# Kernel optimization log

Measured on AMD Instinct MI355X. Metric: run time of the kernel, lower is better.

The kernel has to match this reference:

```python
import jax, jax.numpy as jnp
import numpy as np

V, E, H, L, F, NQ, C = 32000, 256, 8, 4, 1024, 256, 10
B, S = 8, 1024
DK = E // H


def setup_inputs() -> dict:
    key = jax.random.key(0)
    ks = jax.random.split(key, 10)
    f = lambda k, shape, s=0.02: jax.random.normal(k, shape, jnp.float32) * s
    return {
        'tokens': jax.random.randint(ks[0], (B, S), 0, V, jnp.int32),
        'emb': f(ks[1], (V, E), 1.0),
        'theta_attn': f(ks[2], (L, H, DK), 0.5),
        'Wc': f(ks[3], (L, E, E)),
        'bc': jnp.zeros((L, E), jnp.float32),
        'g1': jnp.ones((L, E), jnp.float32),
        'bn1': jnp.zeros((L, E), jnp.float32),
        'theta_ffn': f(ks[4], (L, NQ), 0.5),
        'W1': f(ks[5], (L, NQ, F)),
        'b1': jnp.zeros((L, F), jnp.float32),
        'W2': f(ks[6], (L, F, E)),
        'b2': jnp.zeros((L, E), jnp.float32),
        'g2': jnp.ones((L, E), jnp.float32),
        'bn2': jnp.zeros((L, E), jnp.float32),
        'Wcls': f(ks[7], (E, C)),
        'bcls': jnp.zeros((C,), jnp.float32),
    }


def _ln(x, g, b, eps=1e-5):
    m = x.mean(-1, keepdims=True)
    v = ((x - m) ** 2).mean(-1, keepdims=True)
    return (x - m) / jnp.sqrt(v + eps) * g + b


def _pos_encoding(seq, dim):
    pos = jnp.arange(seq, dtype=jnp.float32)[:, None]
    div = jnp.exp(jnp.arange(0, dim, 2, dtype=jnp.float32) * (-np.log(10000.0) / dim))
    pe = jnp.zeros((seq, dim), jnp.float32)
    pe = pe.at[:, 0::2].set(jnp.sin(pos * div)).at[:, 1::2].set(jnp.cos(pos * div))
    return pe


def _qattn_proj(xh, theta):
    # xh: [B,S,H,dk], theta: [H,dk]. Circuit RX(x+th) per wire, CNOT ring, <Z_i>.
    # Analytic: <Z_i> = prod_{j<=i} cos(phi_j) for i>=1; <Z_0> = prod_{j>=1} cos(phi_j)
    c = jnp.cos(xh + theta)              # [B,S,H,dk]
    cum = jnp.cumprod(c, axis=-1)        # cum[...,i] = prod_{j<=i} c_j
    head0 = jnp.prod(c[..., 1:], axis=-1, keepdims=True)
    return jnp.concatenate([head0, cum[..., 1:]], axis=-1)  # [B,S,H,dk]


def _forward(tokens, emb, theta_attn, Wc, bc, g1, bn1, theta_ffn, W1, b1, W2, b2, g2, bn2, Wcls, bcls):
    b, s = tokens.shape
    x = emb[tokens] + _pos_encoding(s, E)  # [B,S,E]
    scale = 1.0 / np.sqrt(DK)
    for l in range(L):
        # quantum multi-head projection; q = k = v (same deterministic circuit)
        xh = x.reshape(b, s, H, DK)
        p = _qattn_proj(xh, theta_attn[l]).reshape(b, s, E)
        scores = jax.nn.softmax(jnp.einsum('bqe,bke->bqk', p, p) * scale, axis=-1)
        attn = jnp.einsum('bqk,bke->bqe', scores, p) @ Wc[l] + bc[l]
        x = _ln(x + attn, g1[l], bn1[l])
        # quantum FFN: <Z_i> = cos(x_i) * cos(theta_i), NQ == E here
        q = jnp.cos(x[..., :NQ]) * jnp.cos(theta_ffn[l])
        f = jax.nn.relu(q @ W1[l] + b1[l]) @ W2[l] + b2[l]
        x = _ln(x + f, g2[l], bn2[l])
    return x.mean(axis=1) @ Wcls + bcls  # [B,C]


def reference(tokens, emb, theta_attn, Wc, bc, g1, bn1, theta_ffn, W1, b1, W2, b2, g2, bn2, Wcls, bcls):
    return _forward(tokens, emb, theta_attn, Wc, bc, g1, bn1, theta_ffn, W1, b1, W2, b2, g2, bn2, Wcls, bcls)
```

## Files before the change

kernel.cpp:

```cpp
#include <hip/hip_runtime.h>
#include <hip/hip_bf16.h>
#include <math.h>

#define BB 8
#define SS 1024
#define EE 256
#define HH 8
#define DKK 32
#define LL 4
#define FF 1024
#define NQQ 256
#define CC 10

typedef __attribute__((ext_vector_type(8))) short short8;
typedef __attribute__((ext_vector_type(4))) short s16x4;
typedef __attribute__((ext_vector_type(4))) float f32x4;

static __device__ __forceinline__ f32x4 mfma16(short8 a, short8 b, f32x4 c) {
    return __builtin_amdgcn_mfma_f32_16x16x32_bf16(a, b, c, 0, 0, 0);
}
static __device__ __forceinline__ short f2bf(float f) {
    __hip_bfloat16 h = __float2bfloat16(f);
    return *reinterpret_cast<short*>(&h);
}

#define FRAG(P, tile, KG, kg, l) ((P) + (((size_t)((tile)*(KG) + (kg)))*64 + (l))*8)

static __device__ __forceinline__ void qproj_row(
        const float* __restrict__ xrow,
        const float* __restrict__ th,
        int b, int s, int h,
        short* __restrict__ PQ, short* __restrict__ PT) {
    float v[DKK];
    float cum = __cosf(xrow[h * DKK + 0] + th[0]);
    float prod1 = 1.0f;
    #pragma unroll
    for (int j = 1; j < DKK; ++j) {
        float c = __cosf(xrow[h * DKK + j] + th[j]);
        cum *= c;
        prod1 *= c;
        v[j] = cum;
    }
    v[0] = prod1;
    short* pq = PQ + (size_t)b * SS * EE;
    int stile = s >> 4, lr = s & 15;
    #pragma unroll
    for (int lg = 0; lg < 4; ++lg) {
        short8 u;
        #pragma unroll
        for (int j = 0; j < 8; ++j) u[j] = f2bf(v[lg*8 + j]);
        *(short8*)FRAG(pq, stile*8 + h, 1, 0, lg*16 + lr) = u;
    }
    short* pt = PT + (size_t)b * SS * EE;
    int kt = s >> 5, lgs = (s >> 3) & 3, j0 = s & 7;
    #pragma unroll
    for (int j = 0; j < DKK; ++j) {
        int e = h * DKK + j;
        FRAG(pt, e >> 4, 32, kt, lgs*16 + (e & 15))[j0] = f2bf(v[j]);
    }
}

__global__ __launch_bounds__(512) void k_embedq(
        const int* __restrict__ tokens, const float* __restrict__ emb,
        const float* __restrict__ theta_q,
        float* __restrict__ x, short* __restrict__ PQ, short* __restrict__ PT) {
    const int t = threadIdx.x;
    const int bsw = blockIdx.x & 7, local = blockIdx.x >> 3;
    const int tok0 = bsw * SS + local * 32;
    __shared__ float xls[32 * 268];
    {
        int r = t >> 4, c0 = (t & 15) * 16;
        int bs = tok0 + r;
        int s  = bs & (SS - 1);
        int tok = tokens[bs];
        const float* er = emb + (size_t)tok * EE + c0;
        float vals[16];
        #pragma unroll
        for (int i = 0; i < 16; ++i) {
            int col = c0 + i;
            int i2 = col >> 1;
            float div = __expf(-(float)(2 * i2) * (logf(10000.0f) / (float)EE));
            float ang = (float)s * div;
            float pe = (col & 1) ? __cosf(ang) : __sinf(ang);
            vals[i] = er[i] + pe;
            xls[r * 268 + col] = vals[i];
        }
        float* xg = x + (size_t)bs * EE + c0;
        #pragma unroll
        for (int i4 = 0; i4 < 4; ++i4)
            *(float4*)(xg + i4 * 4) = *(const float4*)&vals[i4 * 4];
    }
    __syncthreads();
    if (t < 256) {
        int sl = t >> 3, h = t & 7;
        int bs = tok0 + sl;
        qproj_row(&xls[sl * 268], theta_q + h * DKK,
                  bs >> 10, bs & (SS - 1), h, PQ, PT);
    }
}

__global__ __launch_bounds__(256) void k_trall(
        const float* __restrict__ W1, const float* __restrict__ W2,
        const float* __restrict__ Wc,
        short* __restrict__ W1P, short* __restrict__ W2P, short* __restrict__ WcP) {
    int bid = blockIdx.x;
    int lyr = bid / 576, rem = bid % 576;
    const float* in; short* out; int R, C, tile;
    if (rem < 256)      { in = W1 + (size_t)lyr*NQQ*FF; out = W1P + (size_t)lyr*FF*NQQ; R = NQQ; C = FF;  tile = rem; }
    else if (rem < 512) { in = W2 + (size_t)lyr*FF*EE;  out = W2P + (size_t)lyr*EE*FF;  R = FF;  C = EE;  tile = rem - 256; }
    else                { in = Wc + (size_t)lyr*EE*EE;  out = WcP + (size_t)lyr*EE*EE;  R = EE;  C = EE;  tile = rem - 512; }
    const int KG = R >> 5;
    int tiles_c = C >> 5;
    int tc = tile % tiles_c, tr = tile / tiles_c;
    __shared__ float tl[32][33];
    int t = threadIdx.x;
    int rr = t >> 5, cc = t & 31;
    #pragma unroll
    for (int i = 0; i < 4; ++i)
        tl[rr + i*8][cc] = in[(size_t)(tr*32 + rr + i*8) * C + tc*32 + cc];
    __syncthreads();
    int ro = t >> 3, co = (t & 7) * 4;
    int n = tc*32 + ro;
    int k = tr*32 + co;
    int ntile = n >> 4, lr = n & 15;
    int kg = k >> 5, lg = (k & 31) >> 3, j0 = k & 7;
    s16x4 v;
    v[0] = f2bf(tl[co + 0][ro]);
    v[1] = f2bf(tl[co + 1][ro]);
    v[2] = f2bf(tl[co + 2][ro]);
    v[3] = f2bf(tl[co + 3][ro]);
    *(s16x4*)(FRAG(out, ntile, KG, kg, lg*16 + lr) + j0) = v;
}

__global__ __launch_bounds__(256) void k_attn7(const short* __restrict__ PQ,
                                               const short* __restrict__ PT,
                                               short* __restrict__ YP) {
    const int b   = blockIdx.x & 7;
    const int qt  = blockIdx.x >> 3;
    const int tid = threadIdx.x;
    const int w   = tid >> 6;
    const int l   = tid & 63;
    const int lr  = l & 15, lg = l >> 4;
    const short* pq = PQ + (size_t)b * SS * EE;
    const short* pt = PT + (size_t)b * SS * EE;

    __shared__ float accP[2][16][264];
    __shared__ float lsL[4][16];
    __shared__ short wlds[4][16 * 40];

    short8 qf[8];
    #pragma unroll
    for (int kg = 0; kg < 8; ++kg)
        qf[kg] = *(const short8*)FRAG(pq, qt*8 + kg, 1, 0, l);

    f32x4 acc[16];
    #pragma unroll
    for (int i = 0; i < 16; ++i) acc[i] = f32x4{0.f, 0.f, 0.f, 0.f};
    float ls[4] = {0.f, 0.f, 0.f, 0.f};
    const float scale = 0.17677669529663687f;
    short* wl = wlds[w];

    for (int i = 0; i < 8; ++i) {
        const int kt = w + 4 * i;
        short8 sb0[8], sb1[8];
        #pragma unroll
        for (int kg = 0; kg < 8; ++kg) {
            sb0[kg] = *(const short8*)FRAG(pq, (2*kt)*8   + kg, 1, 0, l);
            sb1[kg] = *(const short8*)FRAG(pq, (2*kt+1)*8 + kg, 1, 0, l);
        }
        f32x4 s0a = {0.f,0.f,0.f,0.f}, s0b = {0.f,0.f,0.f,0.f};
        f32x4 s1a = {0.f,0.f,0.f,0.f}, s1b = {0.f,0.f,0.f,0.f};
        #pragma unroll
        for (int kg = 0; kg < 4; ++kg) {
            s0a = mfma16(qf[kg], sb0[kg], s0a);
            s1a = mfma16(qf[kg], sb1[kg], s1a);
        }
        #pragma unroll
        for (int kg = 4; kg < 8; ++kg) {
            s0b = mfma16(qf[kg], sb0[kg], s0b);
            s1b = mfma16(qf[kg], sb1[kg], s1b);
        }
        short8 pvb0[8];
        #pragma unroll
        for (int nt = 0; nt < 8; ++nt)
            pvb0[nt] = *(const short8*)FRAG(pt, nt, 32, kt, l);

        #pragma unroll
        for (int r = 0; r < 4; ++r) {
            float p0 = __expf((s0a[r] + s0b[r]) * scale);
            float p1 = __expf((s1a[r] + s1b[r]) * scale);
            ls[r] += p0 + p1;
            int q = lg * 4 + r;
            wl[q * 40 + lr]      = f2bf(p0);
            wl[q * 40 + 16 + lr] = f2bf(p1);
        }
        short8 pa = *(const short8*)(wl + lr * 40 + lg * 8);
        short8 pvb1[8];
        #pragma unroll
        for (int nt = 0; nt < 8; ++nt)
            pvb1[nt] = *(const short8*)FRAG(pt, 8 + nt, 32, kt, l);
        #pragma unroll
        for (int nt = 0; nt < 8; ++nt)
            acc[nt] = mfma16(pa, pvb0[nt], acc[nt]);
        #pragma unroll
        for (int nt = 0; nt < 8; ++nt)
            acc[8 + nt] = mfma16(pa, pvb1[nt], acc[8 + nt]);
    }

    #pragma unroll
    for (int r = 0; r < 4; ++r) {
        ls[r] += __shfl_xor(ls[r], 1);
        ls[r] += __shfl_xor(ls[r], 2);
        ls[r] += __shfl_xor(ls[r], 4);
        ls[r] += __shfl_xor(ls[r], 8);
    }
    if (lr == 0) {
        #pragma unroll
        for (int r = 0; r < 4; ++r)
            lsL[w][lg * 4 + r] = ls[r];
    }

    if (w >= 2) {
        #pragma unroll
        for (int nt = 0; nt < 16; ++nt)
            #pragma unroll
            for (int r = 0; r < 4; ++r)
                accP[w - 2][lg * 4 + r][nt * 16 + lr] = acc[nt][r];
    }
    __syncthreads();
    if (w < 2) {
        #pragma unroll
        for (int nt = 0; nt < 16; ++nt)
            #pragma unroll
            for (int r = 0; r < 4; ++r)
                accP[w][lg * 4 + r][nt * 16 + lr] += acc[nt][r];
    }
    __syncthreads();

    const int q = tid >> 4, c = tid & 15;
    float L = lsL[0][q] + lsL[1][q] + lsL[2][q] + lsL[3][q];
    float inv = 1.0f / L;
    short ov[16];
    #pragma unroll
    for (int j = 0; j < 4; ++j) {
        float4 a  = *(const float4*)&accP[0][q][c * 16 + j * 4];
        float4 bb = *(const float4*)&accP[1][q][c * 16 + j * 4];
        ov[j*4 + 0] = f2bf((a.x + bb.x) * inv);
        ov[j*4 + 1] = f2bf((a.y + bb.y) * inv);
        ov[j*4 + 2] = f2bf((a.z + bb.z) * inv);
        ov[j*4 + 3] = f2bf((a.w + bb.w) * inv);
    }
    short* yb = YP + (size_t)b * SS * EE;
    int kgo = c >> 1, lgo = (c & 1) * 2;
    *(short8*)FRAG(yb, qt*8 + kgo, 1, 0, lgo*16 + q)     = *(const short8*)&ov[0];
    *(short8*)FRAG(yb, qt*8 + kgo, 1, 0, (lgo+1)*16 + q) = *(const short8*)&ov[8];
}

__global__ __launch_bounds__(512) void k_wcffnq(
        const short* __restrict__ YP, const short* __restrict__ WcP,
        const float* __restrict__ bc, const float* __restrict__ g1,
        const float* __restrict__ bn1,
        const float* __restrict__ tf, const short* __restrict__ W1P,
        const float* __restrict__ b1, const short* __restrict__ W2P,
        const float* __restrict__ b2, const float* __restrict__ g2,
        const float* __restrict__ bn2,
        float* __restrict__ x,
        const float* __restrict__ theta_q, short* __restrict__ PQ,
        short* __restrict__ PT, int has_next) {
    const int t = threadIdx.x, w = t >> 6, l = t & 63;
    const int lr = l & 15, lg = l >> 4;
    const int wg = w >> 2, wn = w & 3;
    const int b = blockIdx.x & 7;
    const int local = blockIdx.x >> 3;
    const int tok0 = b * SS + local * 32;
    const int qt0 = local * 2;

    __shared__ __align__(16) char smem[34304 + 16384 + 16384];
    float* outw = (float*)smem;
    char*  qls  = smem + 34304;
    char*  hls  = smem + 34304 + 16384;
    float* fout = (float*)(smem + 34304);

    const short* yb = YP + (size_t)b * SS * EE;

    {
        short8 af[8];
        #pragma unroll
        for (int kg = 0; kg < 8; ++kg)
            af[kg] = *(const short8*)FRAG(yb, (qt0 + wg)*8 + kg, 1, 0, l);
        f32x4 acc[4];
        #pragma unroll
        for (int i = 0; i < 4; ++i) acc[i] = f32x4{0.f,0.f,0.f,0.f};
        #pragma unroll
        for (int nt = 0; nt < 4; ++nt) {
            #pragma unroll
            for (int kg = 0; kg < 8; ++kg) {
                short8 bv = *(const short8*)FRAG(WcP, wn*4 + nt, 8, kg, l);
                acc[nt] = mfma16(af[kg], bv, acc[nt]);
            }
        }
        #pragma unroll
        for (int nt = 0; nt < 4; ++nt) {
            int e = wn * 64 + nt * 16 + lr;
            float bce = bc[e];
            #pragma unroll
            for (int r = 0; r < 4; ++r)
                outw[(wg*16 + lg*4 + r) * 268 + e] = acc[nt][r] + bce;
        }
    }
    __syncthreads();

    #pragma unroll
    for (int j = 0; j < 4; ++j) {
        int q = w * 4 + j;
        float4 v  = *(float4*)&outw[q * 268 + l * 4];
        float4 xv = *(const float4*)(x + (size_t)(tok0 + q) * EE + l * 4);
        v.x += xv.x; v.y += xv.y; v.z += xv.z; v.w += xv.w;
        float s = v.x + v.y + v.z + v.w;
        for (int off = 32; off > 0; off >>= 1) s += __shfl_xor(s, off);
        float mean = s * (1.0f / EE);
        float4 d;
        d.x = v.x - mean; d.y = v.y - mean; d.z = v.z - mean; d.w = v.w - mean;
        float s2 = d.x*d.x + d.y*d.y + d.z*d.z + d.w*d.w;
        for (int off = 32; off > 0; off >>= 1) s2 += __shfl_xor(s2, off);
        float inv = rsqrtf(s2 * (1.0f / EE) + 1e-5f);
        float4 gv  = *(const float4*)(g1  + l * 4);
        float4 bnv = *(const float4*)(bn1 + l * 4);
        float4 o;
        o.x = d.x * inv * gv.x + bnv.x;
        o.y = d.y * inv * gv.y + bnv.y;
        o.z = d.z * inv * gv.z + bnv.z;
        o.w = d.w * inv * gv.w + bnv.w;
        *(float4*)&outw[q * 268 + l * 4] = o;
        float4 tv = *(const float4*)(tf + l * 4);
        float q0 = __cosf(o.x) * __cosf(tv.x);
        float q1 = __cosf(o.y) * __cosf(tv.y);
        float q2 = __cosf(o.z) * __cosf(tv.z);
        float q3 = __cosf(o.w) * __cosf(tv.w);
        int byte = (q * 512 + l * 8) ^ ((q & 7) << 4);
        *(unsigned*)(qls + byte) =
            (unsigned)(unsigned short)f2bf(q0) | ((unsigned)(unsigned short)f2bf(q1) << 16);
        *(unsigned*)(qls + byte + 4) =
            (unsigned)(unsigned short)f2bf(q2) | ((unsigned)(unsigned short)f2bf(q3) << 16);
    }
    __syncthreads();

    f32x4 acc2[2][2];
    #pragma unroll
    for (int mt = 0; mt < 2; ++mt)
        #pragma unroll
        for (int nt = 0; nt < 2; ++nt) acc2[mt][nt] = f32x4{0.f,0.f,0.f,0.f};

    for (int fc = 0; fc < 4; ++fc) {
        f32x4 acc1[2][2];
        #pragma unroll
        for (int mt = 0; mt < 2; ++mt)
            #pragma unroll
            for (int i = 0; i < 2; ++i) acc1[mt][i] = f32x4{0.f,0.f,0.f,0.f};
        #pragma unroll
        for (int kg = 0; kg < 8; ++kg) {
            int ca = (kg*32 + lg*8) * 2;
            short8 a0 = *(const short8*)(qls + ((lr*512      + ca) ^ ((lr & 7) << 4)));
            short8 a1 = *(const short8*)(qls + (((16+lr)*512 + ca) ^ ((lr & 7) << 4)));
            #pragma unroll
            for (int i = 0; i < 2; ++i) {
                short8 bv = *(const short8*)FRAG(W1P, fc*16 + w*2 + i, 8, kg, l);
                acc1[0][i] = mfma16(a0, bv, acc1[0][i]);
                acc1[1][i] = mfma16(a1, bv, acc1[1][i]);
            }
        }
        #pragma unroll
        for (int mt = 0; mt < 2; ++mt) {
            #pragma unroll
            for (int i = 0; i < 2; ++i) {
                int fg   = (fc*16 + w*2 + i) * 16 + lr;
                int fcol = (w*2 + i) * 16 + lr;
                float bb = b1[fg];
                #pragma unroll
                for (int r = 0; r < 4; ++r) {
                    int tq = mt * 16 + lg * 4 + r;
                    float hv = fmaxf(acc1[mt][i][r] + bb, 0.0f);
                    int byte = (tq * 512 + fcol * 2) ^ ((tq & 7) << 4);
                    *(short*)(hls + byte) = f2bf(hv);
                }
            }
        }
        __syncthreads();
        #pragma unroll
        for (int k8 = 0; k8 < 8; ++k8) {
            int ca = (k8*32 + lg*8) * 2;
            short8 h0 = *(const short8*)(hls + ((lr*512      + ca) ^ ((lr & 7) << 4)));
            short8 h1 = *(const short8*)(hls + (((16+lr)*512 + ca) ^ ((lr & 7) << 4)));
            #pragma unroll
            for (int nt = 0; nt < 2; ++nt) {
                short8 bv = *(const short8*)FRAG(W2P, w*2 + nt, 32, fc*8 + k8, l);
                acc2[0][nt] = mfma16(h0, bv, acc2[0][nt]);
                acc2[1][nt] = mfma16(h1, bv, acc2[1][nt]);
            }
        }
        __syncthreads();
    }

    #pragma unroll
    for (int mt = 0; mt < 2; ++mt) {
        #pragma unroll
        for (int nt = 0; nt < 2; ++nt) {
            int e = (w*2 + nt) * 16 + lr;
            float b2e = b2[e];
            #pragma unroll
            for (int r = 0; r < 4; ++r)
                fout[(mt*16 + lg*4 + r) * 256 + e] = acc2[mt][nt][r] + b2e;
        }
    }
    __syncthreads();

    #pragma unroll
    for (int j = 0; j < 4; ++j) {
        int q = w * 4 + j;
        float4 v  = *(float4*)&fout[q * 256 + l * 4];
        float4 x1 = *(float4*)&outw[q * 268 + l * 4];
        v.x += x1.x; v.y += x1.y; v.z += x1.z; v.w += x1.w;
        float s = v.x + v.y + v.z + v.w;
        for (int off = 32; off > 0; off >>= 1) s += __shfl_xor(s, off);
        float mean = s * (1.0f / EE);
        float4 d;
        d.x = v.x - mean; d.y = v.y - mean; d.z = v.z - mean; d.w = v.w - mean;
        float s2 = d.x*d.x + d.y*d.y + d.z*d.z + d.w*d.w;
        for (int off = 32; off > 0; off >>= 1) s2 += __shfl_xor(s2, off);
        float inv = rsqrtf(s2 * (1.0f / EE) + 1e-5f);
        float4 gv  = *(const float4*)(g2  + l * 4);
        float4 bnv = *(const float4*)(bn2 + l * 4);
        float4 o;
        o.x = d.x * inv * gv.x + bnv.x;
        o.y = d.y * inv * gv.y + bnv.y;
        o.z = d.z * inv * gv.z + bnv.z;
        o.w = d.w * inv * gv.w + bnv.w;
        *(float4*)(x + (size_t)(tok0 + q) * EE + l * 4) = o;
        *(float4*)&outw[q * 268 + l * 4] = o;
    }
    __syncthreads();

    if (has_next && t < 256) {
        int sl = t >> 3, h = t & 7;
        int bs = tok0 + sl;
        qproj_row(&outw[sl * 268], theta_q + h * DKK,
                  bs >> 10, bs & (SS - 1), h, PQ, PT);
    }
}

__global__ __launch_bounds__(256) void k_head1(const float* __restrict__ x,
                                               float* __restrict__ hpart) {
    int b = blockIdx.x & 7, ch = blockIdx.x >> 3;
    int t = threadIdx.x;
    float acc = 0.0f;
    #pragma unroll 8
    for (int s = ch * 32; s < ch * 32 + 32; ++s)
        acc += x[((size_t)b * SS + s) * EE + t];
    hpart[(size_t)(b * 32 + ch) * EE + t] = acc;
}

__global__ __launch_bounds__(256) void k_head2(const float* __restrict__ hpart,
                                               const float* __restrict__ Wcls,
                                               const float* __restrict__ bcls,
                                               float* __restrict__ out) {
    int b = blockIdx.x;
    int t = threadIdx.x;
    __shared__ float xm[EE];
    float acc = 0.0f;
    #pragma unroll 8
    for (int j = 0; j < 32; ++j)
        acc += hpart[(size_t)(b * 32 + j) * EE + t];
    xm[t] = acc * (1.0f / (float)SS);
    __syncthreads();
    if (t < CC) {
        float a = bcls[t];
        #pragma unroll 8
        for (int e = 0; e < EE; ++e) a += xm[e] * Wcls[e * CC + t];
        out[b * CC + t] = a;
    }
}

extern "C" void kernel_launch(void* const* d_in, const int* in_sizes, int n_in,
                              void* d_out, int out_size, void* d_ws, size_t ws_size,
                              hipStream_t stream) {
    (void)in_sizes; (void)n_in; (void)out_size; (void)ws_size;
    const int*   tokens     = (const int*)d_in[0];
    const float* emb        = (const float*)d_in[1];
    const float* theta_attn = (const float*)d_in[2];
    const float* Wc         = (const float*)d_in[3];
    const float* bc         = (const float*)d_in[4];
    const float* g1         = (const float*)d_in[5];
    const float* bn1        = (const float*)d_in[6];
    const float* theta_ffn  = (const float*)d_in[7];
    const float* W1         = (const float*)d_in[8];
    const float* b1         = (const float*)d_in[9];
    const float* W2         = (const float*)d_in[10];
    const float* b2         = (const float*)d_in[11];
    const float* g2         = (const float*)d_in[12];
    const float* bn2        = (const float*)d_in[13];
    const float* Wcls       = (const float*)d_in[14];
    const float* bcls       = (const float*)d_in[15];
    float* out = (float*)d_out;

    const size_t nTok = (size_t)BB * SS * EE;
    float* x     = (float*)d_ws;
    short* PQ    = (short*)(x + nTok);
    short* PT    = PQ  + nTok;
    short* YP    = PT  + nTok;
    short* W1P   = YP  + nTok;
    short* W2P   = W1P + (size_t)LL * FF * NQQ;
    short* WcP   = W2P + (size_t)LL * EE * FF;
    float* hpart = (float*)(WcP + (size_t)LL * EE * EE);

    k_embedq<<<(BB * SS) / 32, 512, 0, stream>>>(tokens, emb, theta_attn, x, PQ, PT);
    k_trall<<<LL * 576, 256, 0, stream>>>(W1, W2, Wc, W1P, W2P, WcP);

    for (int l = 0; l < LL; ++l) {
        int has_next = (l + 1 < LL) ? 1 : 0;
        const float* thq = theta_attn + (size_t)(has_next ? l + 1 : 0) * HH * DKK;
        k_attn7<<<BB * 64, 256, 0, stream>>>(PQ, PT, YP);
        k_wcffnq<<<(BB * SS) / 32, 512, 0, stream>>>(
            YP, WcP + (size_t)l * EE * EE, bc + (size_t)l * EE,
            g1 + (size_t)l * EE, bn1 + (size_t)l * EE,
            theta_ffn + (size_t)l * NQQ,
            W1P + (size_t)l * FF * NQQ, b1 + (size_t)l * FF,
            W2P + (size_t)l * EE * FF, b2 + (size_t)l * EE,
            g2 + (size_t)l * EE, bn2 + (size_t)l * EE,
            x, thq, PQ, PT, has_next);
    }

    k_head1<<<BB * 32, 256, 0, stream>>>(x, hpart);
    k_head2<<<BB, 256, 0, stream>>>(hpart, Wcls, bcls, out);
}
```

Measured before the change: 248.4 us.

## Merge prep kernels, double-buffer attention K loads, fuse mean-pool into last layer

Merges the embedding/projection kernel and the weight-transpose kernel into one launch, with the embedding part now handling 16 tokens per 256-thread block. The attention loop is unrolled through a macro that prefetches the next key tile's fragments into alternate register buffers while the current tile is computed, and it loads the PV fragments inline. The last layer's FFN kernel computes the per-chunk sequence partial sums from shared memory and skips writing x, which removes the separate head1 kernel. The double buffering raises register pressure in the attention kernel, which could lower occupancy.

```diff
diff --git a/kernel.cpp b/kernel.cpp
--- a/kernel.cpp
+++ b/kernel.cpp
@@ -60,77 +60,117 @@
     }
 }
 
-__global__ __launch_bounds__(512) void k_embedq(
+__global__ __launch_bounds__(256) void k_prep(
+        const float* __restrict__ W1, const float* __restrict__ W2,
+        const float* __restrict__ Wc,
+        short* __restrict__ W1P, short* __restrict__ W2P, short* __restrict__ WcP,
         const int* __restrict__ tokens, const float* __restrict__ emb,
         const float* __restrict__ theta_q,
         float* __restrict__ x, short* __restrict__ PQ, short* __restrict__ PT) {
+    __shared__ float shmem[16 * 268];
     const int t = threadIdx.x;
-    const int bsw = blockIdx.x & 7, local = blockIdx.x >> 3;
-    const int tok0 = bsw * SS + local * 32;
-    __shared__ float xls[32 * 268];
-    {
-        int r = t >> 4, c0 = (t & 15) * 16;
-        int bs = tok0 + r;
-        int s  = bs & (SS - 1);
-        int tok = tokens[bs];
-        const float* er = emb + (size_t)tok * EE + c0;
-        float vals[16];
-        #pragma unroll
-        for (int i = 0; i < 16; ++i) {
-            int col = c0 + i;
-            int i2 = col >> 1;
-            float div = __expf(-(float)(2 * i2) * (logf(10000.0f) / (float)EE));
-            float ang = (float)s * div;
-            float pe = (col & 1) ? __cosf(ang) : __sinf(ang);
-            vals[i] = er[i] + pe;
-            xls[r * 268 + col] = vals[i];
-        }
-        float* xg = x + (size_t)bs * EE + c0;
-        #pragma unroll
-        for (int i4 = 0; i4 < 4; ++i4)
-            *(float4*)(xg + i4 * 4) = *(const float4*)&vals[i4 * 4];
-    }
-    __syncthreads();
-    if (t < 256) {
-        int sl = t >> 3, h = t & 7;
-        int bs = tok0 + sl;
-        qproj_row(&xls[sl * 268], theta_q + h * DKK,
-                  bs >> 10, bs & (SS - 1), h, PQ, PT);
-    }
-}
-
-__global__ __launch_bounds__(256) void k_trall(
-        const float* __restrict__ W1, const float* __restrict__ W2,
-        const float* __restrict__ Wc,
-        short* __restrict__ W1P, short* __restrict__ W2P, short* __restrict__ WcP) {
-    int bid = blockIdx.x;
-    int lyr = bid / 576, rem = bid % 576;
-    const float* in; short* out; int R, C, tile;
-    if (rem < 256)      { in = W1 + (size_t)lyr*NQQ*FF; out = W1P + (size_t)lyr*FF*NQQ; R = NQQ; C = FF;  tile = rem; }
-    else if (rem < 512) { in = W2 + (size_t)lyr*FF*EE;  out = W2P + (size_t)lyr*EE*FF;  R = FF;  C = EE;  tile = rem - 256; }
-    else                { in = Wc + (size_t)lyr*EE*EE;  out = WcP + (size_t)lyr*EE*EE;  R = EE;  C = EE;  tile = rem - 512; }
-    const int KG = R >> 5;
-    int tiles_c = C >> 5;
-    int tc = tile % tiles_c, tr = tile / tiles_c;
-    __shared__ float tl[32][33];
-    int t = threadIdx.x;
-    int rr = t >> 5, cc = t & 31;
-    #pragma unroll
-    for (int i = 0; i < 4; ++i)
-        tl[rr + i*8][cc] = in[(size_t)(tr*32 + rr + i*8) * C + tc*32 + cc];
-    __syncthreads();
-    int ro = t >> 3, co = (t & 7) * 4;
-    int n = tc*32 + ro;
-    int k = tr*32 + co;
-    int ntile = n >> 4, lr = n & 15;
-    int kg = k >> 5, lg = (k & 31) >> 3, j0 = k & 7;
-    s16x4 v;
-    v[0] = f2bf(tl[co + 0][ro]);
-    v[1] = f2bf(tl[co + 1][ro]);
-    v[2] = f2bf(tl[co + 2][ro]);
-    v[3] = f2bf(tl[co + 3][ro]);
-    *(s16x4*)(FRAG(out, ntile, KG, kg, lg*16 + lr) + j0) = v;
-}
+    if (blockIdx.x < 2304) {
+        int bid = blockIdx.x;
+        int lyr = bid / 576, rem = bid % 576;
+        const float* in; short* out; int R, C, tile;
+        if (rem < 256)      { in = W1 + (size_t)lyr*NQQ*FF; out = W1P + (size_t)lyr*FF*NQQ; R = NQQ; C = FF;  tile = rem; }
+        else if (rem < 512) { in = W2 + (size_t)lyr*FF*EE;  out = W2P + (size_t)lyr*EE*FF;  R = FF;  C = EE;  tile = rem - 256; }
+        else                { in = Wc + (size_t)lyr*EE*EE;  out = WcP + (size_t)lyr*EE*EE;  R = EE;  C = EE;  tile = rem - 512; }
+        const int KG = R >> 5;
+        int tiles_c = C >> 5;
+        int tc = tile % tiles_c, tr = tile / tiles_c;
+        float (*tl)[33] = (float(*)[33])shmem;
+        int rr = t >> 5, cc = t & 31;
+        #pragma unroll
+        for (int i = 0; i < 4; ++i)
+            tl[rr + i*8][cc] = in[(size_t)(tr*32 + rr + i*8) * C + tc*32 + cc];
+        __syncthreads();
+        int ro = t >> 3, co = (t & 7) * 4;
+        int n = tc*32 + ro;
+        int k = tr*32 + co;
+        int ntile = n >> 4, lr = n & 15;
+        int kg = k >> 5, lg = (k & 31) >> 3, j0 = k & 7;
+        s16x4 v;
+        v[0] = f2bf(tl[co + 0][ro]);
+        v[1] = f2bf(tl[co + 1][ro]);
+        v[2] = f2bf(tl[co + 2][ro]);
+        v[3] = f2bf(tl[co + 3][ro]);
+        *(s16x4*)(FRAG(out, ntile, KG, kg, lg*16 + lr) + j0) = v;
+    } else {
+        int blk = blockIdx.x - 2304;
+        int bsw = blk & 7, local = blk >> 3;
+        int tok0 = bsw * SS + local * 16;
+        {
+            int r = t >> 4, c0 = (t & 15) * 16;
+            int bs = tok0 + r;
+            int s  = bs & (SS - 1);
+            int tok = tokens[bs];
+            const float* er = emb + (size_t)tok * EE + c0;
+            float vals[16];
+            #pragma unroll
+            for (int i = 0; i < 16; ++i) {
+                int col = c0 + i;
+                int i2 = col >> 1;
+                float div = __expf(-(float)(2 * i2) * (logf(10000.0f) / (float)EE));
+                float ang = (float)s * div;
+                float pe = (col & 1) ? __cosf(ang) : __sinf(ang);
+                vals[i] = er[i] + pe;
+                shmem[r * 268 + col] = vals[i];
+            }
+            float* xg = x + (size_t)bs * EE + c0;
+            #pragma unroll
+            for (int i4 = 0; i4 < 4; ++i4)
+                *(float4*)(xg + i4 * 4) = *(const float4*)&vals[i4 * 4];
+        }
+        __syncthreads();
+        if (t < 128) {
+            int sl = t >> 3, h = t & 7;
+            int bs = tok0 + sl;
+            qproj_row(&shmem[sl * 268], theta_q + h * DKK,
+                      bs >> 10, bs & (SS - 1), h, PQ, PT);
+        }
+    }
+}
+
+#define ATTN_STEP(I, C0, C1, N0, N1)                                          \
+    {                                                                         \
+        const int kt = w + 4 * (I);                                           \
+        if ((I) < 7) {                                                        \
+            const int ktn = kt + 4;                                           \
+            _Pragma("unroll")                                                 \
+            for (int kg = 0; kg < 8; ++kg) {                                  \
+                N0[kg] = *(const short8*)FRAG(pq, (2*ktn)*8   + kg, 1, 0, l); \
+                N1[kg] = *(const short8*)FRAG(pq, (2*ktn+1)*8 + kg, 1, 0, l); \
+            }                                                                 \
+        }                                                                     \
+        f32x4 s0a = {0.f,0.f,0.f,0.f}, s0b = {0.f,0.f,0.f,0.f};               \
+        f32x4 s1a = {0.f,0.f,0.f,0.f}, s1b = {0.f,0.f,0.f,0.f};               \
+        _Pragma("unroll")                                                     \
+        for (int kg = 0; kg < 4; ++kg) {                                      \
+            s0a = mfma16(qf[kg], C0[kg], s0a);                                \
+            s1a = mfma16(qf[kg], C1[kg], s1a);                                \
+        }                                                                     \
+        _Pragma("unroll")                                                     \
+        for (int kg = 4; kg < 8; ++kg) {                                      \
+            s0b = mfma16(qf[kg], C0[kg], s0b);                                \
+            s1b = mfma16(qf[kg], C1[kg], s1b);                                \
+        }                                                                     \
+        _Pragma("unroll")                                                     \
+        for (int r = 0; r < 4; ++r) {                                         \
+            float p0 = __expf((s0a[r] + s0b[r]) * scale);                     \
+            float p1 = __expf((s1a[r] + s1b[r]) * scale);                     \
+            ls[r] += p0 + p1;                                                 \
+            int qq = lg * 4 + r;                                              \
+            wl[qq * 40 + lr]      = f2bf(p0);                                 \
+            wl[qq * 40 + 16 + lr] = f2bf(p1);                                 \
+        }                                                                     \
+        short8 pa = *(const short8*)(wl + lr * 40 + lg * 8);                  \
+        _Pragma("unroll")                                                     \
+        for (int nt = 0; nt < 16; ++nt) {                                     \
+            short8 bv = *(const short8*)FRAG(pt, nt, 32, kt, l);              \
+            acc[nt] = mfma16(pa, bv, acc[nt]);                                \
+        }                                                                     \
+    }
 
 __global__ __launch_bounds__(256) void k_attn7(const short* __restrict__ PQ,
                                                const short* __restrict__ PT,
@@ -160,52 +200,21 @@
     const float scale = 0.17677669529663687f;
     short* wl = wlds[w];
 
-    for (int i = 0; i < 8; ++i) {
-        const int kt = w + 4 * i;
-        short8 sb0[8], sb1[8];
-        #pragma unroll
-        for (int kg = 0; kg < 8; ++kg) {
-            sb0[kg] = *(const short8*)FRAG(pq, (2*kt)*8   + kg, 1, 0, l);
-            sb1[kg] = *(const short8*)FRAG(pq, (2*kt+1)*8 + kg, 1, 0, l);
-        }
-        f32x4 s0a = {0.f,0.f,0.f,0.f}, s0b = {0.f,0.f,0.f,0.f};
-        f32x4 s1a = {0.f,0.f,0.f,0.f}, s1b = {0.f,0.f,0.f,0.f};
-        #pragma unroll
-        for (int kg = 0; kg < 4; ++kg) {
-            s0a = mfma16(qf[kg], sb0[kg], s0a);
-            s1a = mfma16(qf[kg], sb1[kg], s1a);
-        }
-        #pragma unroll
-        for (int kg = 4; kg < 8; ++kg) {
-            s0b = mfma16(qf[kg], sb0[kg], s0b);
-            s1b = mfma16(qf[kg], sb1[kg], s1b);
-        }
-        short8 pvb0[8];
-        #pragma unroll
-        for (int nt = 0; nt < 8; ++nt)
-            pvb0[nt] = *(const short8*)FRAG(pt, nt, 32, kt, l);
-
-        #pragma unroll
-        for (int r = 0; r < 4; ++r) {
-            float p0 = __expf((s0a[r] + s0b[r]) * scale);
-            float p1 = __expf((s1a[r] + s1b[r]) * scale);
-            ls[r] += p0 + p1;
-            int q = lg * 4 + r;
-            wl[q * 40 + lr]      = f2bf(p0);
-            wl[q * 40 + 16 + lr] = f2bf(p1);
-        }
-        short8 pa = *(const short8*)(wl + lr * 40 + lg * 8);
-        short8 pvb1[8];
-        #pragma unroll
-        for (int nt = 0; nt < 8; ++nt)
-            pvb1[nt] = *(const short8*)FRAG(pt, 8 + nt, 32, kt, l);
-        #pragma unroll
-        for (int nt = 0; nt < 8; ++nt)
-            acc[nt] = mfma16(pa, pvb0[nt], acc[nt]);
-        #pragma unroll
-        for (int nt = 0; nt < 8; ++nt)
-            acc[8 + nt] = mfma16(pa, pvb1[nt], acc[8 + nt]);
-    }
+    short8 sbA0[8], sbA1[8], sbB0[8], sbB1[8];
+    #pragma unroll
+    for (int kg = 0; kg < 8; ++kg) {
+        sbA0[kg] = *(const short8*)FRAG(pq, (2*w)*8   + kg, 1, 0, l);
+        sbA1[kg] = *(const short8*)FRAG(pq, (2*w+1)*8 + kg, 1, 0, l);
+    }
+
+    ATTN_STEP(0, sbA0, sbA1, sbB0, sbB1)
+    ATTN_STEP(1, sbB0, sbB1, sbA0, sbA1)
+    ATTN_STEP(2, sbA0, sbA1, sbB0, sbB1)
+    ATTN_STEP(3, sbB0, sbB1, sbA0, sbA1)
+    ATTN_STEP(4, sbA0, sbA1, sbB0, sbB1)
+    ATTN_STEP(5, sbB0, sbB1, sbA0, sbA1)
+    ATTN_STEP(6, sbA0, sbA1, sbB0, sbB1)
+    ATTN_STEP(7, sbB0, sbB1, sbA0, sbA1)
 
     #pragma unroll
     for (int r = 0; r < 4; ++r) {
@@ -266,7 +275,7 @@
         const float* __restrict__ bn2,
         float* __restrict__ x,
         const float* __restrict__ theta_q, short* __restrict__ PQ,
-        short* __restrict__ PT, int has_next) {
+        short* __restrict__ PT, float* __restrict__ hpart, int has_next) {
     const int t = threadIdx.x, w = t >> 6, l = t & 63;
     const int lr = l & 15, lg = l >> 4;
     const int wg = w >> 2, wn = w & 3;
@@ -435,28 +444,28 @@
         o.y = d.y * inv * gv.y + bnv.y;
         o.z = d.z * inv * gv.z + bnv.z;
         o.w = d.w * inv * gv.w + bnv.w;
-        *(float4*)(x + (size_t)(tok0 + q) * EE + l * 4) = o;
+        if (has_next)
+            *(float4*)(x + (size_t)(tok0 + q) * EE + l * 4) = o;
         *(float4*)&outw[q * 268 + l * 4] = o;
     }
     __syncthreads();
 
-    if (has_next && t < 256) {
-        int sl = t >> 3, h = t & 7;
-        int bs = tok0 + sl;
-        qproj_row(&outw[sl * 268], theta_q + h * DKK,
-                  bs >> 10, bs & (SS - 1), h, PQ, PT);
-    }
-}
-
-__global__ __launch_bounds__(256) void k_head1(const float* __restrict__ x,
-                                               float* __restrict__ hpart) {
-    int b = blockIdx.x & 7, ch = blockIdx.x >> 3;
-    int t = threadIdx.x;
-    float acc = 0.0f;
-    #pragma unroll 8
-    for (int s = ch * 32; s < ch * 32 + 32; ++s)
-        acc += x[((size_t)b * SS + s) * EE + t];
-    hpart[(size_t)(b * 32 + ch) * EE + t] = acc;
+    if (has_next) {
+        if (t < 256) {
+            int sl = t >> 3, h = t & 7;
+            int bs = tok0 + sl;
+            qproj_row(&outw[sl * 268], theta_q + h * DKK,
+                      bs >> 10, bs & (SS - 1), h, PQ, PT);
+        }
+    } else {
+        if (t < 256) {
+            float acc = 0.0f;
+            #pragma unroll 8
+            for (int r = 0; r < 32; ++r)
+                acc += outw[r * 268 + t];
+            hpart[(size_t)(b * 32 + local) * EE + t] = acc;
+        }
+    }
 }
 
 __global__ __launch_bounds__(256) void k_head2(const float* __restrict__ hpart,
@@ -512,8 +521,8 @@
     short* WcP   = W2P + (size_t)LL * EE * FF;
     float* hpart = (float*)(WcP + (size_t)LL * EE * EE);
 
-    k_embedq<<<(BB * SS) / 32, 512, 0, stream>>>(tokens, emb, theta_attn, x, PQ, PT);
-    k_trall<<<LL * 576, 256, 0, stream>>>(W1, W2, Wc, W1P, W2P, WcP);
+    k_prep<<<2304 + 512, 256, 0, stream>>>(
+        W1, W2, Wc, W1P, W2P, WcP, tokens, emb, theta_attn, x, PQ, PT);
 
     for (int l = 0; l < LL; ++l) {
         int has_next = (l + 1 < LL) ? 1 : 0;
@@ -526,9 +535,8 @@
             W1P + (size_t)l * FF * NQQ, b1 + (size_t)l * FF,
             W2P + (size_t)l * EE * FF, b2 + (size_t)l * EE,
             g2 + (size_t)l * EE, bn2 + (size_t)l * EE,
-            x, thq, PQ, PT, has_next);
-    }
-
-    k_head1<<<BB * 32, 256, 0, stream>>>(x, hpart);
+            x, thq, PQ, PT, hpart, has_next);
+    }
+
     k_head2<<<BB, 256, 0, stream>>>(hpart, Wcls, bcls, out);
 }
```

Result: no change. 253.0 us (+1.9%).

## Merge prep kernels, fuse head reduction into last layer, add MFMA priority hints

Applied to the files above, without the earlier changes.

Combines the embedding/projection kernel and the weight-transpose kernel into one launch, with the embedding part now using 16-token blocks. The last layer's FFN kernel now writes per-block column sums straight to hpart, which removes the k_head1 launch and the final store of x. It also wraps the MFMA loops in attention and FFN with s_setprio raises to favour matrix issue. The aim is fewer launches and less global traffic. The risk is smaller embed blocks and priority hints that may not help scheduling.

```diff
diff --git a/kernel.cpp b/kernel.cpp
--- a/kernel.cpp
+++ b/kernel.cpp
@@ -60,76 +60,76 @@
     }
 }
 
-__global__ __launch_bounds__(512) void k_embedq(
+__global__ __launch_bounds__(256) void k_prep(
+        const float* __restrict__ W1, const float* __restrict__ W2,
+        const float* __restrict__ Wc,
+        short* __restrict__ W1P, short* __restrict__ W2P, short* __restrict__ WcP,
         const int* __restrict__ tokens, const float* __restrict__ emb,
         const float* __restrict__ theta_q,
         float* __restrict__ x, short* __restrict__ PQ, short* __restrict__ PT) {
+    __shared__ float shmem[16 * 268];
     const int t = threadIdx.x;
-    const int bsw = blockIdx.x & 7, local = blockIdx.x >> 3;
-    const int tok0 = bsw * SS + local * 32;
-    __shared__ float xls[32 * 268];
-    {
-        int r = t >> 4, c0 = (t & 15) * 16;
-        int bs = tok0 + r;
-        int s  = bs & (SS - 1);
-        int tok = tokens[bs];
-        const float* er = emb + (size_t)tok * EE + c0;
-        float vals[16];
-        #pragma unroll
-        for (int i = 0; i < 16; ++i) {
-            int col = c0 + i;
-            int i2 = col >> 1;
-            float div = __expf(-(float)(2 * i2) * (logf(10000.0f) / (float)EE));
-            float ang = (float)s * div;
-            float pe = (col & 1) ? __cosf(ang) : __sinf(ang);
-            vals[i] = er[i] + pe;
-            xls[r * 268 + col] = vals[i];
-        }
-        float* xg = x + (size_t)bs * EE + c0;
-        #pragma unroll
-        for (int i4 = 0; i4 < 4; ++i4)
-            *(float4*)(xg + i4 * 4) = *(const float4*)&vals[i4 * 4];
-    }
-    __syncthreads();
-    if (t < 256) {
-        int sl = t >> 3, h = t & 7;
-        int bs = tok0 + sl;
-        qproj_row(&xls[sl * 268], theta_q + h * DKK,
-                  bs >> 10, bs & (SS - 1), h, PQ, PT);
-    }
-}
-
-__global__ __launch_bounds__(256) void k_trall(
-        const float* __restrict__ W1, const float* __restrict__ W2,
-        const float* __restrict__ Wc,
-        short* __restrict__ W1P, short* __restrict__ W2P, short* __restrict__ WcP) {
-    int bid = blockIdx.x;
-    int lyr = bid / 576, rem = bid % 576;
-    const float* in; short* out; int R, C, tile;
-    if (rem < 256)      { in = W1 + (size_t)lyr*NQQ*FF; out = W1P + (size_t)lyr*FF*NQQ; R = NQQ; C = FF;  tile = rem; }
-    else if (rem < 512) { in = W2 + (size_t)lyr*FF*EE;  out = W2P + (size_t)lyr*EE*FF;  R = FF;  C = EE;  tile = rem - 256; }
-    else                { in = Wc + (size_t)lyr*EE*EE;  out = WcP + (size_t)lyr*EE*EE;  R = EE;  C = EE;  tile = rem - 512; }
-    const int KG = R >> 5;
-    int tiles_c = C >> 5;
-    int tc = tile % tiles_c, tr = tile / tiles_c;
-    __shared__ float tl[32][33];
-    int t = threadIdx.x;
-    int rr = t >> 5, cc = t & 31;
-    #pragma unroll
-    for (int i = 0; i < 4; ++i)
-        tl[rr + i*8][cc] = in[(size_t)(tr*32 + rr + i*8) * C + tc*32 + cc];
-    __syncthreads();
-    int ro = t >> 3, co = (t & 7) * 4;
-    int n = tc*32 + ro;
-    int k = tr*32 + co;
-    int ntile = n >> 4, lr = n & 15;
-    int kg = k >> 5, lg = (k & 31) >> 3, j0 = k & 7;
-    s16x4 v;
-    v[0] = f2bf(tl[co + 0][ro]);
-    v[1] = f2bf(tl[co + 1][ro]);
-    v[2] = f2bf(tl[co + 2][ro]);
-    v[3] = f2bf(tl[co + 3][ro]);
-    *(s16x4*)(FRAG(out, ntile, KG, kg, lg*16 + lr) + j0) = v;
+    if (blockIdx.x < 2304) {
+        int bid = blockIdx.x;
+        int lyr = bid / 576, rem = bid % 576;
+        const float* in; short* out; int R, C, tile;
+        if (rem < 256)      { in = W1 + (size_t)lyr*NQQ*FF; out = W1P + (size_t)lyr*FF*NQQ; R = NQQ; C = FF;  tile = rem; }
+        else if (rem < 512) { in = W2 + (size_t)lyr*FF*EE;  out = W2P + (size_t)lyr*EE*FF;  R = FF;  C = EE;  tile = rem - 256; }
+        else                { in = Wc + (size_t)lyr*EE*EE;  out = WcP + (size_t)lyr*EE*EE;  R = EE;  C = EE;  tile = rem - 512; }
+        const int KG = R >> 5;
+        int tiles_c = C >> 5;
+        int tc = tile % tiles_c, tr = tile / tiles_c;
+        float (*tl)[33] = (float(*)[33])shmem;
+        int rr = t >> 5, cc = t & 31;
+        #pragma unroll
+        for (int i = 0; i < 4; ++i)
+            tl[rr + i*8][cc] = in[(size_t)(tr*32 + rr + i*8) * C + tc*32 + cc];
+        __syncthreads();
+        int ro = t >> 3, co = (t & 7) * 4;
+        int n = tc*32 + ro;
+        int k = tr*32 + co;
+        int ntile = n >> 4, lr = n & 15;
+        int kg = k >> 5, lg = (k & 31) >> 3, j0 = k & 7;
+        s16x4 v;
+        v[0] = f2bf(tl[co + 0][ro]);
+        v[1] = f2bf(tl[co + 1][ro]);
+        v[2] = f2bf(tl[co + 2][ro]);
+        v[3] = f2bf(tl[co + 3][ro]);
+        *(s16x4*)(FRAG(out, ntile, KG, kg, lg*16 + lr) + j0) = v;
+    } else {
+        int blk = blockIdx.x - 2304;
+        int bsw = blk & 7, local = blk >> 3;
+        int tok0 = bsw * SS + local * 16;
+        {
+            int r = t >> 4, c0 = (t & 15) * 16;
+            int bs = tok0 + r;
+            int s  = bs & (SS - 1);
+            int tok = tokens[bs];
+            const float* er = emb + (size_t)tok * EE + c0;
+            float vals[16];
+            #pragma unroll
+            for (int i = 0; i < 16; ++i) {
+                int col = c0 + i;
+                int i2 = col >> 1;
+                float div = __expf(-(float)(2 * i2) * (logf(10000.0f) / (float)EE));
+                float ang = (float)s * div;
+                float pe = (col & 1) ? __cosf(ang) : __sinf(ang);
+                vals[i] = er[i] + pe;
+                shmem[r * 268 + col] = vals[i];
+            }
+            float* xg = x + (size_t)bs * EE + c0;
+            #pragma unroll
+            for (int i4 = 0; i4 < 4; ++i4)
+                *(float4*)(xg + i4 * 4) = *(const float4*)&vals[i4 * 4];
+        }
+        __syncthreads();
+        if (t < 128) {
+            int sl = t >> 3, h = t & 7;
+            int bs = tok0 + sl;
+            qproj_row(&shmem[sl * 268], theta_q + h * DKK,
+                      bs >> 10, bs & (SS - 1), h, PQ, PT);
+        }
+    }
 }
 
 __global__ __launch_bounds__(256) void k_attn7(const short* __restrict__ PQ,
@@ -170,6 +170,7 @@
         }
         f32x4 s0a = {0.f,0.f,0.f,0.f}, s0b = {0.f,0.f,0.f,0.f};
         f32x4 s1a = {0.f,0.f,0.f,0.f}, s1b = {0.f,0.f,0.f,0.f};
+        __builtin_amdgcn_s_setprio(1);
         #pragma unroll
         for (int kg = 0; kg < 4; ++kg) {
             s0a = mfma16(qf[kg], sb0[kg], s0a);
@@ -180,6 +181,7 @@
             s0b = mfma16(qf[kg], sb0[kg], s0b);
             s1b = mfma16(qf[kg], sb1[kg], s1b);
         }
+        __builtin_amdgcn_s_setprio(0);
         short8 pvb0[8];
         #pragma unroll
         for (int nt = 0; nt < 8; ++nt)
@@ -199,12 +201,14 @@
         #pragma unroll
         for (int nt = 0; nt < 8; ++nt)
             pvb1[nt] = *(const short8*)FRAG(pt, 8 + nt, 32, kt, l);
+        __builtin_amdgcn_s_setprio(1);
         #pragma unroll
         for (int nt = 0; nt < 8; ++nt)
             acc[nt] = mfma16(pa, pvb0[nt], acc[nt]);
         #pragma unroll
         for (int nt = 0; nt < 8; ++nt)
             acc[8 + nt] = mfma16(pa, pvb1[nt], acc[8 + nt]);
+        __builtin_amdgcn_s_setprio(0);
     }
 
     #pragma unroll
@@ -266,7 +270,7 @@
         const float* __restrict__ bn2,
         float* __restrict__ x,
         const float* __restrict__ theta_q, short* __restrict__ PQ,
-        short* __restrict__ PT, int has_next) {
+        short* __restrict__ PT, float* __restrict__ hpart, int has_next) {
     const int t = threadIdx.x, w = t >> 6, l = t & 63;
     const int lr = l & 15, lg = l >> 4;
     const int wg = w >> 2, wn = w & 3;
@@ -291,6 +295,7 @@
         f32x4 acc[4];
         #pragma unroll
         for (int i = 0; i < 4; ++i) acc[i] = f32x4{0.f,0.f,0.f,0.f};
+        __builtin_amdgcn_s_setprio(1);
         #pragma unroll
         for (int nt = 0; nt < 4; ++nt) {
             #pragma unroll
@@ -299,6 +304,7 @@
                 acc[nt] = mfma16(af[kg], bv, acc[nt]);
             }
         }
+        __builtin_amdgcn_s_setprio(0);
         #pragma unroll
         for (int nt = 0; nt < 4; ++nt) {
             int e = wn * 64 + nt * 16 + lr;
@@ -357,6 +363,7 @@
         for (int mt = 0; mt < 2; ++mt)
             #pragma unroll
             for (int i = 0; i < 2; ++i) acc1[mt][i] = f32x4{0.f,0.f,0.f,0.f};
+        __builtin_amdgcn_s_setprio(1);
         #pragma unroll
         for (int kg = 0; kg < 8; ++kg) {
             int ca = (kg*32 + lg*8) * 2;
@@ -369,6 +376,7 @@
                 acc1[1][i] = mfma16(a1, bv, acc1[1][i]);
             }
         }
+        __builtin_amdgcn_s_setprio(0);
         #pragma unroll
         for (int mt = 0; mt < 2; ++mt) {
             #pragma unroll
@@ -386,6 +394,7 @@
             }
         }
         __syncthreads();
+        __builtin_amdgcn_s_setprio(1);
         #pragma unroll
         for (int k8 = 0; k8 < 8; ++k8) {
             int ca = (k8*32 + lg*8) * 2;
@@ -398,6 +407,7 @@
                 acc2[1][nt] = mfma16(h1, bv, acc2[1][nt]);
             }
         }
+        __builtin_amdgcn_s_setprio(0);
         __syncthreads();
     }
 
@@ -435,28 +445,28 @@
         o.y = d.y * inv * gv.y + bnv.y;
         o.z = d.z * inv * gv.z + bnv.z;
         o.w = d.w * inv * gv.w + bnv.w;
-        *(float4*)(x + (size_t)(tok0 + q) * EE + l * 4) = o;
+        if (has_next)
+            *(float4*)(x + (size_t)(tok0 + q) * EE + l * 4) = o;
         *(float4*)&outw[q * 268 + l * 4] = o;
     }
     __syncthreads();
 
-    if (has_next && t < 256) {
-        int sl = t >> 3, h = t & 7;
-        int bs = tok0 + sl;
-        qproj_row(&outw[sl * 268], theta_q + h * DKK,
-                  bs >> 10, bs & (SS - 1), h, PQ, PT);
-    }
-}
-
-__global__ __launch_bounds__(256) void k_head1(const float* __restrict__ x,
-                                               float* __restrict__ hpart) {
-    int b = blockIdx.x & 7, ch = blockIdx.x >> 3;
-    int t = threadIdx.x;
-    float acc = 0.0f;
-    #pragma unroll 8
-    for (int s = ch * 32; s < ch * 32 + 32; ++s)
-        acc += x[((size_t)b * SS + s) * EE + t];
-    hpart[(size_t)(b * 32 + ch) * EE + t] = acc;
+    if (has_next) {
+        if (t < 256) {
+            int sl = t >> 3, h = t & 7;
+            int bs = tok0 + sl;
+            qproj_row(&outw[sl * 268], theta_q + h * DKK,
+                      bs >> 10, bs & (SS - 1), h, PQ, PT);
+        }
+    } else {
+        if (t < 256) {
+            float acc = 0.0f;
+            #pragma unroll 8
+            for (int r = 0; r < 32; ++r)
+                acc += outw[r * 268 + t];
+            hpart[(size_t)(b * 32 + local) * EE + t] = acc;
+        }
+    }
 }
 
 __global__ __launch_bounds__(256) void k_head2(const float* __restrict__ hpart,
@@ -512,8 +522,8 @@
     short* WcP   = W2P + (size_t)LL * EE * FF;
     float* hpart = (float*)(WcP + (size_t)LL * EE * EE);
 
-    k_embedq<<<(BB * SS) / 32, 512, 0, stream>>>(tokens, emb, theta_attn, x, PQ, PT);
-    k_trall<<<LL * 576, 256, 0, stream>>>(W1, W2, Wc, W1P, W2P, WcP);
+    k_prep<<<2304 + 512, 256, 0, stream>>>(
+        W1, W2, Wc, W1P, W2P, WcP, tokens, emb, theta_attn, x, PQ, PT);
 
     for (int l = 0; l < LL; ++l) {
         int has_next = (l + 1 < LL) ? 1 : 0;
@@ -526,9 +536,8 @@
             W1P + (size_t)l * FF * NQQ, b1 + (size_t)l * FF,
             W2P + (size_t)l * EE * FF, b2 + (size_t)l * EE,
             g2 + (size_t)l * EE, bn2 + (size_t)l * EE,
-            x, thq, PQ, PT, has_next);
-    }
-
-    k_head1<<<BB * 32, 256, 0, stream>>>(x, hpart);
+            x, thq, PQ, PT, hpart, has_next);
+    }
+
     k_head2<<<BB, 256, 0, stream>>>(hpart, Wcls, bcls, out);
 }
```

Result: slower. 281.5 us (+13.4%).
